# Kernel optimization log

Measured on AMD Instinct MI355X. Metric: run time of the kernel, lower is better.

Reference implementation:

```python
import jax, jax.numpy as jnp
from jax import lax
import numpy as np

NPOINT, RADIUS, NSAMPLE = 1024, 0.2, 32
MLP, IN_CH, EPS = (64, 64, 128), 6, 1e-5
B, N = 8, 4096


def farthest_point_sample(xyz, npoint):
    # xyz: [B, N, 3] -> idx [B, npoint]. Deterministic start at index 0.
    Bn, Nn, _ = xyz.shape
    def body(carry, _):
        dist, farthest = carry  # dist [B,N], farthest [B]
        centroid = jnp.take_along_axis(xyz, farthest[:, None, None], axis=1)  # [B,1,3]
        d = jnp.sum((xyz - centroid) ** 2, axis=-1)  # [B,N]
        dist = jnp.minimum(dist, d)
        return (dist, jnp.argmax(dist, axis=-1).astype(jnp.int32)), farthest
    init = (jnp.full((Bn, Nn), 1e10, xyz.dtype), jnp.zeros((Bn,), jnp.int32))
    _, idx = lax.scan(body, init, None, length=npoint)  # [npoint, B]
    return idx.T


def query_ball_point(radius, nsample, xyz, new_xyz):
    # xyz [B,N,3], new_xyz [B,S,3] -> idx [B,S,nsample]
    Bn, Nn, _ = xyz.shape
    sq = (jnp.sum(new_xyz ** 2, -1)[:, :, None]
          + jnp.sum(xyz ** 2, -1)[:, None, :]
          - 2.0 * jnp.einsum('bsc,bnc->bsn', new_xyz, xyz))  # [B,S,N]
    gidx = jnp.where(sq > radius ** 2, Nn, jnp.arange(Nn, dtype=jnp.int32)[None, None, :])
    gidx = jnp.sort(gidx, axis=-1)[:, :, :nsample]
    first = gidx[:, :, :1]
    return jnp.where(gidx == Nn, first, gidx)


def setup_inputs():
    key = jax.random.key(0)
    ks = jax.random.split(key, 8)
    inp = {
        'xyz': jax.random.uniform(ks[0], (B, 3, N), dtype=jnp.float32),
        'points': jax.random.normal(ks[1], (B, 3, N), dtype=jnp.float32),
    }
    last = IN_CH
    for i, oc in enumerate(MLP):
        inp[f'w{i}'] = jax.random.normal(ks[2 + i], (oc, last), dtype=jnp.float32) * 0.1
        inp[f'b{i}'] = jnp.zeros((oc,), jnp.float32)
        inp[f'g{i}'] = jnp.ones((oc,), jnp.float32)
        inp[f'be{i}'] = jnp.zeros((oc,), jnp.float32)
        last = oc
    return inp


def reference(xyz, points, w0, b0, g0, be0, w1, b1, g1, be1, w2, b2, g2, be2):
    x = jnp.transpose(xyz, (0, 2, 1))      # [B,N,3]
    p = jnp.transpose(points, (0, 2, 1))   # [B,N,D]
    fidx = farthest_point_sample(x, NPOINT)                       # [B,S]
    new_xyz = jnp.take_along_axis(x, fidx[:, :, None], axis=1)    # [B,S,3]
    idx = query_ball_point(RADIUS, NSAMPLE, x, new_xyz)           # [B,S,K]
    gather = jax.vmap(lambda a, i: a[i])                          # per-batch gather
    grouped_xyz = gather(x, idx)                                  # [B,S,K,3]
    grouped_xyz_norm = grouped_xyz - new_xyz[:, :, None, :]
    grouped_points = gather(p, idx)                               # [B,S,K,D]
    feat = jnp.concatenate([grouped_xyz_norm, grouped_points], axis=-1)  # [B,S,K,C]
    for w, b, g, be in ((w0, b0, g0, be0), (w1, b1, g1, be1), (w2, b2, g2, be2)):
        feat = jnp.einsum('bskc,oc->bsko', feat, w) + b
        mean = feat.mean(axis=(0, 1, 2))
        var = feat.var(axis=(0, 1, 2))
        feat = (feat - mean) * lax.rsqrt(var + EPS) * g + be  # BatchNorm (training stats)
        feat = jax.nn.relu(feat)
    new_points = jnp.max(feat, axis=2)                            # max over K -> [B,S,Cout]
    return jnp.transpose(new_xyz, (0, 2, 1)), jnp.transpose(new_points, (0, 2, 1))
```

## Files before the change

### kernel.cpp

```cpp
#include <hip/hip_runtime.h>
#include <stdint.h>

#define NPTS   4096
#define NPOINT 1024
#define NSAMP  32
#define NROWS  262144
#define RAD2   0.04f

typedef float v2f __attribute__((ext_vector_type(2)));
typedef __attribute__((ext_vector_type(8))) short bf16x8;
typedef __attribute__((ext_vector_type(4))) float f32x4;

__device__ __forceinline__ unsigned short f2bf(float x) {
    unsigned u = __float_as_uint(x);
    return (unsigned short)((u + 0x7FFFu + ((u >> 16) & 1u)) >> 16);
}
__device__ __forceinline__ unsigned pack2bf(float a, float b) {
    return (unsigned)f2bf(a) | ((unsigned)f2bf(b) << 16);
}

#define DPPMAX(v, C)                                                           \
    fmaxf(__int_as_float(__builtin_amdgcn_update_dpp(                          \
              0, __float_as_int(v), C, 0xf, 0xf, true)),                       \
          (v))

__global__ __launch_bounds__(256) void fps_kernel(const float* __restrict__ xyz,
                                                  float* __restrict__ outx)
{
    __shared__ __align__(16) float4 pxyz[NPTS];
    __shared__ __align__(16) float4 orec[NPOINT];
    __shared__ __align__(16) unsigned long long wkey[2][4];
    const int b = blockIdx.x, tid = threadIdx.x;
    const int lane = tid & 63, wid = tid >> 6;
    const float* base = xyz + b * 3 * NPTS;

    float Xs[16], Ys[16], Zs[16];
#pragma unroll
    for (int j = 0; j < 16; ++j) {
        const int n = j * 256 + tid;
        Xs[j] = base[n];
        Ys[j] = base[NPTS + n];
        Zs[j] = base[2 * NPTS + n];
        pxyz[n] = make_float4(Xs[j], Ys[j], Zs[j], 0.0f);
    }
    v2f X2[8], Y2[8], Z2[8], D2[8];
#pragma unroll
    for (int j = 0; j < 8; ++j) {
        X2[j] = (v2f){Xs[2 * j], Xs[2 * j + 1]};
        Y2[j] = (v2f){Ys[2 * j], Ys[2 * j + 1]};
        Z2[j] = (v2f){Zs[2 * j], Zs[2 * j + 1]};
        D2[j] = (v2f){1e10f, 1e10f};
    }
    __syncthreads();
    float4 c4 = pxyz[0];
    float cx = c4.x, cy = c4.y, cz = c4.z;

    for (int t = 0; t < NPOINT; ++t) {
        if (tid == 0) orec[t] = make_float4(cx, cy, cz, 0.0f);
        const v2f cxv = (v2f){cx, cx}, cyv = (v2f){cy, cy}, czv = (v2f){cz, cz};
        float bv = -1.0f; int bi = 0;
#pragma unroll
        for (int j = 0; j < 8; ++j) {
            v2f nd;
            {
#pragma clang fp contract(off)
                const v2f dx = X2[j] - cxv;
                const v2f dy = Y2[j] - cyv;
                const v2f dz = Z2[j] - czv;
                const v2f m0 = dx * dx;
                const v2f m1 = dy * dy;
                const v2f m2 = dz * dz;
                const v2f d = (m0 + m1) + m2;
                nd = __builtin_elementwise_min(D2[j], d);
            }
            D2[j] = nd;
            if (nd.x > bv) { bv = nd.x; bi = j * 512 + tid; }
            if (nd.y > bv) { bv = nd.y; bi = j * 512 + 256 + tid; }
        }
        float rv = bv;
        rv = DPPMAX(rv, 0x111);
        rv = DPPMAX(rv, 0x112);
        rv = DPPMAX(rv, 0x114);
        rv = DPPMAX(rv, 0x118);
        rv = DPPMAX(rv, 0x142);
        rv = DPPMAX(rv, 0x143);
        const unsigned wmax =
            (unsigned)__builtin_amdgcn_readlane(__float_as_int(rv), 63);
        unsigned long long mask = __ballot(__float_as_uint(bv) == wmax);
        unsigned best =
            (unsigned)__builtin_amdgcn_readlane(bi, (int)__builtin_ctzll(mask));
        mask &= mask - 1ull;
        while (mask) {
            const unsigned cand = (unsigned)__builtin_amdgcn_readlane(
                bi, (int)__builtin_ctzll(mask));
            best = cand < best ? cand : best;
            mask &= mask - 1ull;
        }
        if (lane == 0)
            wkey[t & 1][wid] = ((unsigned long long)wmax << 32) |
                               (unsigned)(~best);
        __syncthreads();
        const ulonglong2* wk = (const ulonglong2*)wkey[t & 1];
        const ulonglong2 ka = wk[0], kb = wk[1];
        unsigned long long kk = ka.x;
        if (ka.y > kk) kk = ka.y;
        if (kb.x > kk) kk = kb.x;
        if (kb.y > kk) kk = kb.y;
        const int farthest = (int)(~(unsigned)kk) & (NPTS - 1);
        c4 = pxyz[farthest];
        cx = c4.x; cy = c4.y; cz = c4.z;
    }
    __syncthreads();
    float* ox = outx + b * 3 * NPOINT;
    for (int i = tid; i < NPOINT; i += 256) {
        const float4 c = orec[i];
        ox[i]              = c.x;
        ox[NPOINT + i]     = c.y;
        ox[2 * NPOINT + i] = c.z;
    }
}

__global__ __launch_bounds__(256) void ball_kernel(const float* __restrict__ xyz,
                                                   const float* __restrict__ pts,
                                                   const float* __restrict__ outx,
                                                   float* __restrict__ mom,
                                                   uint4* __restrict__ featbuf)
{
    __shared__ float red[4][42];
    __shared__ int smyidx[4][NSAMP];
    const int tid = threadIdx.x;
    const int w = blockIdx.x * 4 + (tid >> 6);
    const int lane = tid & 63, wid = tid >> 6;
    const int b = w >> 10, s = w & 1023;
    const float* base = xyz + b * 3 * NPTS;
    const float cx = outx[b * 3 * NPOINT + s];
    const float cy = outx[b * 3 * NPOINT + NPOINT + s];
    const float cz = outx[b * 3 * NPOINT + 2 * NPOINT + s];
    const float sumS = __fadd_rn(__fadd_rn(__fmul_rn(cx, cx), __fmul_rn(cy, cy)),
                                 __fmul_rn(cz, cz));
    int cnt = 0, first_n = -1;
    int* myidx = smyidx[wid];

    for (int chunk = 0; chunk < NPTS / 64 && cnt < NSAMP; ++chunk) {
        const int n = chunk * 64 + lane;
        float nx = base[n], ny = base[NPTS + n], nz = base[2 * NPTS + n];
        float sumN = __fadd_rn(__fadd_rn(__fmul_rn(nx, nx), __fmul_rn(ny, ny)),
                               __fmul_rn(nz, nz));
        float dot = __fadd_rn(__fadd_rn(__fmul_rn(cx, nx), __fmul_rn(cy, ny)),
                              __fmul_rn(cz, nz));
        float sq = __fsub_rn(__fadd_rn(sumS, sumN), __fmul_rn(2.0f, dot));
        bool keep = (sq <= RAD2);
        unsigned long long mask = __ballot(keep);
        if (first_n < 0 && mask) first_n = chunk * 64 + (int)__builtin_ctzll(mask);
        int pos = cnt + __popcll(mask & ((1ull << lane) - 1ull));
        if (keep && pos < NSAMP) myidx[pos] = n;
        cnt += __popcll(mask);
    }
    if (cnt < NSAMP) {
        if (lane >= cnt && lane < NSAMP) myidx[lane] = first_n;
    }

    float m[42];
#pragma unroll
    for (int i = 0; i < 42; ++i) m[i] = 0.f;
    if (lane < 32) {
        const int idx = myidx[lane];
        const float* pb = pts + b * 3 * NPTS;
        float f[6];
        f[0] = base[idx] - cx;
        f[1] = base[NPTS + idx] - cy;
        f[2] = base[2 * NPTS + idx] - cz;
        f[3] = pb[idx];
        f[4] = pb[NPTS + idx];
        f[5] = pb[2 * NPTS + idx];
        featbuf[w * NSAMP + lane] =
            make_uint4(pack2bf(f[0], f[1]), pack2bf(f[2], f[3]),
                       pack2bf(f[4], f[5]), 0u);
#pragma unroll
        for (int c = 0; c < 6; ++c) m[c] = f[c];
#pragma unroll
        for (int c = 0; c < 6; ++c)
#pragma unroll
            for (int d = 0; d < 6; ++d)
                m[6 + c * 6 + d] = f[c] * f[d];
    }
#pragma unroll
    for (int i = 0; i < 42; ++i) {
        float v = m[i];
        v += __shfl_xor(v, 1);  v += __shfl_xor(v, 2);  v += __shfl_xor(v, 4);
        v += __shfl_xor(v, 8);  v += __shfl_xor(v, 16); v += __shfl_xor(v, 32);
        m[i] = v;
    }
    if (lane == 0) {
#pragma unroll
        for (int i = 0; i < 42; ++i) red[wid][i] = m[i];
    }
    __syncthreads();
    if (tid < 42)
        atomicAdd(&mom[tid], red[0][tid] + red[1][tid] + red[2][tid] + red[3][tid]);
}

__device__ __forceinline__ void compute_bn0(int o, const float* __restrict__ mom,
                                            const float* __restrict__ w0,
                                            const float* __restrict__ g,
                                            const float* __restrict__ be,
                                            float* __restrict__ sbn0)
{
    float w[6];
#pragma unroll
    for (int c = 0; c < 6; ++c) w[c] = w0[o * 6 + c];
    const float inv = 1.0f / (float)NROWS;
    float mean = 0.f;
#pragma unroll
    for (int c = 0; c < 6; ++c) mean = fmaf(w[c], mom[c], mean);
    mean *= inv;
    float ey2 = 0.f;
#pragma unroll
    for (int c = 0; c < 6; ++c) {
        float t = 0.f;
#pragma unroll
        for (int d = 0; d < 6; ++d) t = fmaf(w[d], mom[6 + c * 6 + d], t);
        ey2 = fmaf(w[c], t, ey2);
    }
    ey2 *= inv;
    const float var = ey2 - mean * mean;
    const float scale = g[o] * rsqrtf(var + 1e-5f);
    sbn0[o] = scale;
    sbn0[64 + o] = be[o] - mean * scale;
}

#define XP  72
#define WP  72
#define W0P 40

__global__ __launch_bounds__(256, 2) void mlp1_kernel(
    const uint4* __restrict__ featbuf,
    const float* __restrict__ w0, const float* __restrict__ mom,
    const float* __restrict__ g0, const float* __restrict__ be0,
    const float* __restrict__ w1, float* __restrict__ stats,
    uint4* __restrict__ l1store)
{
    __shared__ __align__(16) unsigned short sw0[64 * W0P];
    __shared__ __align__(16) unsigned short sw1[64 * WP];
    __shared__ __align__(16) unsigned short xb[4][32 * XP];
    __shared__ float sbn0[128];
    __shared__ float red[4][128];
    const int tid = threadIdx.x, lane = tid & 63, wid = tid >> 6;

    for (int i = tid; i < 64 * W0P / 2; i += 256) ((unsigned*)sw0)[i] = 0;
    if (tid < 64) compute_bn0(tid, mom, w0, g0, be0, sbn0);
    __syncthreads();
    for (int i = tid; i < 192; i += 256) {
        const int o = i / 3, c = (i % 3) * 2;
        *(unsigned*)&sw0[o * W0P + c] = pack2bf(w0[o * 6 + c], w0[o * 6 + c + 1]);
    }
    for (int i = tid; i < 2048; i += 256) {
        const int o = i >> 5, k = (i & 31) * 2;
        *(unsigned*)&sw1[o * WP + k] = pack2bf(w1[o * 64 + k], w1[o * 64 + k + 1]);
    }

    const int mh = lane & 15, q = lane >> 4;
    unsigned short* X = xb[wid];
    const int rbase = blockIdx.x * 512 + wid * 32;
    float sA[4] = {0.f, 0.f, 0.f, 0.f}, qA[4] = {0.f, 0.f, 0.f, 0.f};

    for (int c = 0; c < 4; ++c) {
        __syncthreads();
        if (lane < 32) {
            const int r = rbase + c * 128 + lane;
            uint4* xq = (uint4*)&xb[wid][lane * XP];
            xq[0] = featbuf[r];
            xq[1] = make_uint4(0u, 0u, 0u, 0u);
            xq[2] = make_uint4(0u, 0u, 0u, 0u);
            xq[3] = make_uint4(0u, 0u, 0u, 0u);
        }
        __syncthreads();
        f32x4 acc0[2][4] = {};
        {
            bf16x8 a[2], bw[4];
#pragma unroll
            for (int mt = 0; mt < 2; ++mt)
                a[mt] = *(const bf16x8*)&X[(mt * 16 + mh) * XP + q * 8];
#pragma unroll
            for (int nt = 0; nt < 4; ++nt)
                bw[nt] = *(const bf16x8*)&sw0[(nt * 16 + mh) * W0P + q * 8];
#pragma unroll
            for (int mt = 0; mt < 2; ++mt)
#pragma unroll
                for (int nt = 0; nt < 4; ++nt)
                    acc0[mt][nt] = __builtin_amdgcn_mfma_f32_16x16x32_bf16(
                        a[mt], bw[nt], acc0[mt][nt], 0, 0, 0);
        }
        __syncthreads();
#pragma unroll
        for (int nt = 0; nt < 4; ++nt) {
            const int ch = nt * 16 + mh;
            const float sc = sbn0[ch], sh = sbn0[64 + ch];
#pragma unroll
            for (int mt = 0; mt < 2; ++mt)
#pragma unroll
                for (int rr = 0; rr < 4; ++rr) {
                    const float v = fmaxf(fmaf(acc0[mt][nt][rr], sc, sh), 0.0f);
                    X[(mt * 16 + q * 4 + rr) * XP + ch] = f2bf(v);
                }
        }
        __syncthreads();
        f32x4 acc1[2][4] = {};
#pragma unroll
        for (int ks = 0; ks < 2; ++ks) {
            bf16x8 a[2], bw[4];
#pragma unroll
            for (int mt = 0; mt < 2; ++mt)
                a[mt] = *(const bf16x8*)&X[(mt * 16 + mh) * XP + ks * 32 + q * 8];
#pragma unroll
            for (int nt = 0; nt < 4; ++nt)
                bw[nt] = *(const bf16x8*)&sw1[(nt * 16 + mh) * WP + ks * 32 + q * 8];
#pragma unroll
            for (int mt = 0; mt < 2; ++mt)
#pragma unroll
                for (int nt = 0; nt < 4; ++nt)
                    acc1[mt][nt] = __builtin_amdgcn_mfma_f32_16x16x32_bf16(
                        a[mt], bw[nt], acc1[mt][nt], 0, 0, 0);
        }
#pragma unroll
        for (int nt = 0; nt < 4; ++nt)
#pragma unroll
            for (int mt = 0; mt < 2; ++mt)
#pragma unroll
                for (int rr = 0; rr < 4; ++rr) {
                    const float v = acc1[mt][nt][rr];
                    sA[nt] += v;
                    qA[nt] = fmaf(v, v, qA[nt]);
                }
        if (l1store) {
#pragma unroll
            for (int nt = 0; nt < 4; ++nt) {
                const int ch = nt * 16 + mh;
#pragma unroll
                for (int mt = 0; mt < 2; ++mt)
#pragma unroll
                    for (int rr = 0; rr < 4; ++rr)
                        X[(mt * 16 + q * 4 + rr) * XP + ch] =
                            f2bf(acc1[mt][nt][rr]);
            }
            uint4* dst = l1store +
                         (size_t)(blockIdx.x * 16 + c * 4 + wid) * 256;
#pragma unroll
            for (int k = 0; k < 4; ++k) {
                const int idx = lane * 4 + k;
                const int row = idx >> 3, c8 = (idx & 7) * 8;
                dst[idx] = *(const uint4*)&X[row * XP + c8];
            }
        }
    }
#pragma unroll
    for (int nt = 0; nt < 4; ++nt) {
        float s = sA[nt], qq = qA[nt];
        s += __shfl_xor(s, 16); qq += __shfl_xor(qq, 16);
        s += __shfl_xor(s, 32); qq += __shfl_xor(qq, 32);
        if (q == 0) {
            red[wid][nt * 16 + mh] = s;
            red[wid][64 + nt * 16 + mh] = qq;
        }
    }
    __syncthreads();
    if (tid < 128)
        atomicAdd(&stats[tid],
                  red[0][tid] + red[1][tid] + red[2][tid] + red[3][tid]);
}

__global__ __launch_bounds__(256, 2) void mlp2b_kernel(
    const uint4* __restrict__ l1buf,
    const float* __restrict__ stats1,
    const float* __restrict__ g1, const float* __restrict__ be1,
    const float* __restrict__ w2,
    float* __restrict__ stats, float* __restrict__ gmax)
{
    __shared__ __align__(16) unsigned short sw2[128 * WP];
    __shared__ float sbn1[128];
    __shared__ float red[4][256];
    const int tid = threadIdx.x, lane = tid & 63, wid = tid >> 6;

    if (tid < 64) {
        const float inv = 1.0f / (float)NROWS;
        const float mean = stats1[tid] * inv;
        const float var = stats1[64 + tid] * inv - mean * mean;
        const float scale = g1[tid] * rsqrtf(var + 1e-5f);
        sbn1[tid] = scale;
        sbn1[64 + tid] = be1[tid] - mean * scale;
    }
    for (int i = tid; i < 4096; i += 256) {
        const int o = i >> 5, k = (i & 31) * 2;
        *(unsigned*)&sw2[o * WP + k] = pack2bf(w2[o * 64 + k], w2[o * 64 + k + 1]);
    }
    __syncthreads();

    const int mh = lane & 15, q = lane >> 4;
    float sc[2][8], sh[2][8];
#pragma unroll
    for (int ks = 0; ks < 2; ++ks)
#pragma unroll
        for (int j = 0; j < 8; ++j) {
            const int ch = ks * 32 + q * 8 + j;
            sc[ks][j] = sbn1[ch];
            sh[ks][j] = sbn1[64 + ch];
        }

    float sA[8], qA[8];
#pragma unroll
    for (int i = 0; i < 8; ++i) { sA[i] = 0.f; qA[i] = 0.f; }

    for (int c = 0; c < 4; ++c) {
        const int g = blockIdx.x * 16 + c * 4 + wid;
        const uint4* src = l1buf + (size_t)g * 256;
        bf16x8 a2[2][2];
#pragma unroll
        for (int mt = 0; mt < 2; ++mt)
#pragma unroll
            for (int ks = 0; ks < 2; ++ks) {
                const int row = mt * 16 + mh;
                const uint4 v = src[row * 8 + ks * 4 + q];
                const unsigned* pv = (const unsigned*)&v;
                unsigned r[4];
#pragma unroll
                for (int p = 0; p < 4; ++p) {
                    const unsigned u = pv[p];
                    const float f0 = __uint_as_float(u << 16);
                    const float f1 = __uint_as_float(u & 0xFFFF0000u);
                    const float v0 =
                        fmaxf(fmaf(f0, sc[ks][2 * p], sh[ks][2 * p]), 0.0f);
                    const float v1 =
                        fmaxf(fmaf(f1, sc[ks][2 * p + 1], sh[ks][2 * p + 1]),
                              0.0f);
                    r[p] = pack2bf(v0, v1);
                }
                const uint4 packed = make_uint4(r[0], r[1], r[2], r[3]);
                a2[mt][ks] = __builtin_bit_cast(bf16x8, packed);
            }
#pragma unroll
        for (int nt = 0; nt < 8; ++nt) {
            f32x4 acc[2] = {};
#pragma unroll
            for (int ks = 0; ks < 2; ++ks) {
                const bf16x8 bw =
                    *(const bf16x8*)&sw2[(nt * 16 + mh) * WP + ks * 32 + q * 8];
#pragma unroll
                for (int mt = 0; mt < 2; ++mt)
                    acc[mt] = __builtin_amdgcn_mfma_f32_16x16x32_bf16(
                        a2[mt][ks], bw, acc[mt], 0, 0, 0);
            }
            float m = -3.0e38f;
#pragma unroll
            for (int mt = 0; mt < 2; ++mt)
#pragma unroll
                for (int rr = 0; rr < 4; ++rr) {
                    const float v = acc[mt][rr];
                    sA[nt] += v;
                    qA[nt] = fmaf(v, v, qA[nt]);
                    m = fmaxf(m, v);
                }
            m = fmaxf(m, __shfl_xor(m, 16));
            m = fmaxf(m, __shfl_xor(m, 32));
            if (q == 0) gmax[(nt * 16 + mh) * 8192 + g] = m;
        }
    }
#pragma unroll
    for (int nt = 0; nt < 8; ++nt) {
        float s = sA[nt], qq = qA[nt];
        s += __shfl_xor(s, 16); qq += __shfl_xor(qq, 16);
        s += __shfl_xor(s, 32); qq += __shfl_xor(qq, 32);
        if (q == 0) {
            red[wid][nt * 16 + mh] = s;
            red[wid][128 + nt * 16 + mh] = qq;
        }
    }
    __syncthreads();
    atomicAdd(&stats[tid],
              red[0][tid] + red[1][tid] + red[2][tid] + red[3][tid]);
}

__global__ __launch_bounds__(256, 2) void mlp2_kernel(
    const uint4* __restrict__ featbuf,
    const float* __restrict__ w0, const float* __restrict__ mom,
    const float* __restrict__ g0, const float* __restrict__ be0,
    const float* __restrict__ w1, const float* __restrict__ stats1,
    const float* __restrict__ g1, const float* __restrict__ be1,
    const float* __restrict__ w2,
    float* __restrict__ stats, float* __restrict__ gmax)
{
    __shared__ __align__(16) unsigned short sw0[64 * W0P];
    __shared__ __align__(16) unsigned short sw1[64 * WP];
    __shared__ __align__(16) unsigned short sw2[128 * WP];
    __shared__ __align__(16) unsigned short xb[4][32 * XP];
    __shared__ float sbn0[128];
    __shared__ float sbn1[128];
    __shared__ float red[4][256];
    const int tid = threadIdx.x, lane = tid & 63, wid = tid >> 6;

    for (int i = tid; i < 64 * W0P / 2; i += 256) ((unsigned*)sw0)[i] = 0;
    if (tid < 64) {
        compute_bn0(tid, mom, w0, g0, be0, sbn0);
    } else if (tid < 128) {
        const int ch = tid - 64;
        const float inv = 1.0f / (float)NROWS;
        const float mean = stats1[ch] * inv;
        const float var = stats1[64 + ch] * inv - mean * mean;
        const float scale = g1[ch] * rsqrtf(var + 1e-5f);
        sbn1[ch] = scale;
        sbn1[64 + ch] = be1[ch] - mean * scale;
    }
    __syncthreads();
    for (int i = tid; i < 192; i += 256) {
        const int o = i / 3, c = (i % 3) * 2;
        *(unsigned*)&sw0[o * W0P + c] = pack2bf(w0[o * 6 + c], w0[o * 6 + c + 1]);
    }
    for (int i = tid; i < 2048; i += 256) {
        const int o = i >> 5, k = (i & 31) * 2;
        *(unsigned*)&sw1[o * WP + k] = pack2bf(w1[o * 64 + k], w1[o * 64 + k + 1]);
    }
    for (int i = tid; i < 4096; i += 256) {
        const int o = i >> 5, k = (i & 31) * 2;
        *(unsigned*)&sw2[o * WP + k] = pack2bf(w2[o * 64 + k], w2[o * 64 + k + 1]);
    }

    const int mh = lane & 15, q = lane >> 4;
    unsigned short* X = xb[wid];
    const int rbase = blockIdx.x * 512 + wid * 32;
    float sA[8], qA[8];
#pragma unroll
    for (int i = 0; i < 8; ++i) { sA[i] = 0.f; qA[i] = 0.f; }

    for (int c = 0; c < 4; ++c) {
        __syncthreads();
        if (lane < 32) {
            const int r = rbase + c * 128 + lane;
            uint4* xq = (uint4*)&xb[wid][lane * XP];
            xq[0] = featbuf[r];
            xq[1] = make_uint4(0u, 0u, 0u, 0u);
            xq[2] = make_uint4(0u, 0u, 0u, 0u);
            xq[3] = make_uint4(0u, 0u, 0u, 0u);
        }
        __syncthreads();
        f32x4 acc0[2][4] = {};
        {
            bf16x8 a[2], bw[4];
#pragma unroll
            for (int mt = 0; mt < 2; ++mt)
                a[mt] = *(const bf16x8*)&X[(mt * 16 + mh) * XP + q * 8];
#pragma unroll
            for (int nt = 0; nt < 4; ++nt)
                bw[nt] = *(const bf16x8*)&sw0[(nt * 16 + mh) * W0P + q * 8];
#pragma unroll
            for (int mt = 0; mt < 2; ++mt)
#pragma unroll
                for (int nt = 0; nt < 4; ++nt)
                    acc0[mt][nt] = __builtin_amdgcn_mfma_f32_16x16x32_bf16(
                        a[mt], bw[nt], acc0[mt][nt], 0, 0, 0);
        }
        __syncthreads();
#pragma unroll
        for (int nt = 0; nt < 4; ++nt) {
            const int ch = nt * 16 + mh;
            const float sc = sbn0[ch], sh = sbn0[64 + ch];
#pragma unroll
            for (int mt = 0; mt < 2; ++mt)
#pragma unroll
                for (int rr = 0; rr < 4; ++rr) {
                    const float v = fmaxf(fmaf(acc0[mt][nt][rr], sc, sh), 0.0f);
                    X[(mt * 16 + q * 4 + rr) * XP + ch] = f2bf(v);
                }
        }
        __syncthreads();
        f32x4 acc1[2][4] = {};
#pragma unroll
        for (int ks = 0; ks < 2; ++ks) {
            bf16x8 a[2], bw[4];
#pragma unroll
            for (int mt = 0; mt < 2; ++mt)
                a[mt] = *(const bf16x8*)&X[(mt * 16 + mh) * XP + ks * 32 + q * 8];
#pragma unroll
            for (int nt = 0; nt < 4; ++nt)
                bw[nt] = *(const bf16x8*)&sw1[(nt * 16 + mh) * WP + ks * 32 + q * 8];
#pragma unroll
            for (int mt = 0; mt < 2; ++mt)
#pragma unroll
                for (int nt = 0; nt < 4; ++nt)
                    acc1[mt][nt] = __builtin_amdgcn_mfma_f32_16x16x32_bf16(
                        a[mt], bw[nt], acc1[mt][nt], 0, 0, 0);
        }
        __syncthreads();
#pragma unroll
        for (int nt = 0; nt < 4; ++nt) {
            const int ch = nt * 16 + mh;
            const float sc = sbn1[ch], sh = sbn1[64 + ch];
#pragma unroll
            for (int mt = 0; mt < 2; ++mt)
#pragma unroll
                for (int rr = 0; rr < 4; ++rr) {
                    const float v = fmaxf(fmaf(acc1[mt][nt][rr], sc, sh), 0.0f);
                    X[(mt * 16 + q * 4 + rr) * XP + ch] = f2bf(v);
                }
        }
        __syncthreads();
        const int g = blockIdx.x * 16 + c * 4 + wid;
        bf16x8 a2[2][2];
#pragma unroll
        for (int mt = 0; mt < 2; ++mt)
#pragma unroll
            for (int ks = 0; ks < 2; ++ks)
                a2[mt][ks] = *(const bf16x8*)&X[(mt * 16 + mh) * XP + ks * 32 + q * 8];
#pragma unroll
        for (int nt = 0; nt < 8; ++nt) {
            f32x4 acc[2] = {};
#pragma unroll
            for (int ks = 0; ks < 2; ++ks) {
                const bf16x8 bw = *(const bf16x8*)&sw2[(nt * 16 + mh) * WP + ks * 32 + q * 8];
#pragma unroll
                for (int mt = 0; mt < 2; ++mt)
                    acc[mt] = __builtin_amdgcn_mfma_f32_16x16x32_bf16(
                        a2[mt][ks], bw, acc[mt], 0, 0, 0);
            }
            float m = -3.0e38f;
#pragma unroll
            for (int mt = 0; mt < 2; ++mt)
#pragma unroll
                for (int rr = 0; rr < 4; ++rr) {
                    const float v = acc[mt][rr];
                    sA[nt] += v;
                    qA[nt] = fmaf(v, v, qA[nt]);
                    m = fmaxf(m, v);
                }
            m = fmaxf(m, __shfl_xor(m, 16));
            m = fmaxf(m, __shfl_xor(m, 32));
            if (q == 0) gmax[(nt * 16 + mh) * 8192 + g] = m;
        }
    }
#pragma unroll
    for (int nt = 0; nt < 8; ++nt) {
        float s = sA[nt], qq = qA[nt];
        s += __shfl_xor(s, 16); qq += __shfl_xor(qq, 16);
        s += __shfl_xor(s, 32); qq += __shfl_xor(qq, 32);
        if (q == 0) {
            red[wid][nt * 16 + mh] = s;
            red[wid][128 + nt * 16 + mh] = qq;
        }
    }
    __syncthreads();
    atomicAdd(&stats[tid],
              red[0][tid] + red[1][tid] + red[2][tid] + red[3][tid]);
}

__global__ __launch_bounds__(256) void final_kernel(const float* __restrict__ gmax,
                                                    const float* __restrict__ stats2,
                                                    const float* __restrict__ g2,
                                                    const float* __restrict__ be2,
                                                    float* __restrict__ out2)
{
    __shared__ float sbn[256];
    const int tid = threadIdx.x;
    if (tid < 128) {
        const float inv = 1.0f / (float)NROWS;
        const float mean = stats2[tid] * inv;
        const float var = stats2[128 + tid] * inv - mean * mean;
        const float scale = g2[tid] * rsqrtf(var + 1e-5f);
        sbn[tid] = scale;
        sbn[128 + tid] = be2[tid] - mean * scale;
    }
    __syncthreads();
    const int t = blockIdx.x * 256 + tid;
    const int s = t & 1023;
    const int o = (t >> 10) & 127;
    const int b = t >> 17;
    const int g = (b << 10) | s;
    float v = gmax[o * 8192 + g];
    v = fmaf(v, sbn[o], sbn[128 + o]);
    out2[t] = fmaxf(v, 0.0f);
}

extern "C" void kernel_launch(void* const* d_in, const int* in_sizes, int n_in,
                              void* d_out, int out_size, void* d_ws, size_t ws_size,
                              hipStream_t stream)
{
    const float* xyz = (const float*)d_in[0];
    const float* pts = (const float*)d_in[1];
    const float* w0  = (const float*)d_in[2];
    const float* g0  = (const float*)d_in[4];
    const float* be0 = (const float*)d_in[5];
    const float* w1  = (const float*)d_in[6];
    const float* g1  = (const float*)d_in[8];
    const float* be1 = (const float*)d_in[9];
    const float* w2  = (const float*)d_in[10];
    const float* g2  = (const float*)d_in[12];
    const float* be2 = (const float*)d_in[13];

    float* out_xyz = (float*)d_out;
    float* out2    = out_xyz + 8 * 3 * NPOINT;

    char* wsb = (char*)d_ws;
    float* stats   = (float*)(wsb + 32768 + 1048576);
    float* gmax    = stats + 1024;
    uint4* featbuf = (uint4*)(gmax + 128 * 8192);
    uint4* l1buf   = featbuf + NROWS;

    float* mom    = stats;
    float* stats1 = stats + 128;
    float* stats2 = stats + 256;

    const bool bigws = ws_size >= (size_t)43100000;

    hipMemsetAsync(stats, 0, 512 * sizeof(float), stream);

    fps_kernel<<<8, 256, 0, stream>>>(xyz, out_xyz);
    ball_kernel<<<2048, 256, 0, stream>>>(xyz, pts, out_xyz, mom, featbuf);
    if (bigws) {
        mlp1_kernel<<<512, 256, 0, stream>>>(featbuf, w0, mom, g0, be0,
                                             w1, stats1, l1buf);
        mlp2b_kernel<<<512, 256, 0, stream>>>(l1buf, stats1, g1, be1,
                                              w2, stats2, gmax);
    } else {
        mlp1_kernel<<<512, 256, 0, stream>>>(featbuf, w0, mom, g0, be0,
                                             w1, stats1, nullptr);
        mlp2_kernel<<<512, 256, 0, stream>>>(featbuf, w0, mom, g0, be0,
                                             w1, stats1, g1, be1,
                                             w2, stats2, gmax);
    }
    final_kernel<<<4096, 256, 0, stream>>>(gmax, stats2, g2, be2, out2);
}
```

Baseline: 793.3 us.

## Prefetch next chunk loads, use DPP reductions, drop block barriers in MLP loop

The ball-query loop now prefetches the next 64-point chunk's coordinates into registers so global-load latency overlaps the distance test and ballot. The 42-value moment reduction swaps four shuffle-xor steps for DPP row operations. The MLP kernel prefetches the next featbuf tile into a register and replaces the per-iteration __syncthreads calls with one barrier after the weight setup, since each wave works only on its own staging buffer. Removing the barriers assumes same-wave LDS ordering is enough, and the DPP pattern has to reproduce the original butterfly sums exactly.

```diff
diff --git a/kernel.cpp b/kernel.cpp
--- a/kernel.cpp
+++ b/kernel.cpp
@@ -23,6 +23,10 @@
     fmaxf(__int_as_float(__builtin_amdgcn_update_dpp(                          \
               0, __float_as_int(v), C, 0xf, 0xf, true)),                       \
           (v))
+#define DPPADD(v, C)                                                           \
+    (__int_as_float(__builtin_amdgcn_update_dpp(                               \
+         0, __float_as_int(v), C, 0xf, 0xf, true)) +                           \
+     (v))
 
 __global__ __launch_bounds__(256) void fps_kernel(const float* __restrict__ xyz,
                                                   float* __restrict__ outx)
@@ -141,13 +145,18 @@
     int cnt = 0, first_n = -1;
     int* myidx = smyidx[wid];
 
+    float nx = base[lane], ny = base[NPTS + lane], nz = base[2 * NPTS + lane];
     for (int chunk = 0; chunk < NPTS / 64 && cnt < NSAMP; ++chunk) {
+        const float x = nx, y = ny, z = nz;
+        if (chunk + 1 < NPTS / 64) {
+            const int nn = (chunk + 1) * 64 + lane;
+            nx = base[nn]; ny = base[NPTS + nn]; nz = base[2 * NPTS + nn];
+        }
         const int n = chunk * 64 + lane;
-        float nx = base[n], ny = base[NPTS + n], nz = base[2 * NPTS + n];
-        float sumN = __fadd_rn(__fadd_rn(__fmul_rn(nx, nx), __fmul_rn(ny, ny)),
-                               __fmul_rn(nz, nz));
-        float dot = __fadd_rn(__fadd_rn(__fmul_rn(cx, nx), __fmul_rn(cy, ny)),
-                              __fmul_rn(cz, nz));
+        float sumN = __fadd_rn(__fadd_rn(__fmul_rn(x, x), __fmul_rn(y, y)),
+                               __fmul_rn(z, z));
+        float dot = __fadd_rn(__fadd_rn(__fmul_rn(cx, x), __fmul_rn(cy, y)),
+                              __fmul_rn(cz, z));
         float sq = __fsub_rn(__fadd_rn(sumS, sumN), __fmul_rn(2.0f, dot));
         bool keep = (sq <= RAD2);
         unsigned long long mask = __ballot(keep);
@@ -187,8 +196,11 @@
 #pragma unroll
     for (int i = 0; i < 42; ++i) {
         float v = m[i];
-        v += __shfl_xor(v, 1);  v += __shfl_xor(v, 2);  v += __shfl_xor(v, 4);
-        v += __shfl_xor(v, 8);  v += __shfl_xor(v, 16); v += __shfl_xor(v, 32);
+        v = DPPADD(v, 0x111);
+        v = DPPADD(v, 0x112);
+        v = DPPADD(v, 0x114);
+        v = DPPADD(v, 0x118);
+        v += __shfl_xor(v, 16);
         m[i] = v;
     }
     if (lane == 0) {
@@ -258,23 +270,25 @@
         const int o = i >> 5, k = (i & 31) * 2;
         *(unsigned*)&sw1[o * WP + k] = pack2bf(w1[o * 64 + k], w1[o * 64 + k + 1]);
     }
+    __syncthreads();
 
     const int mh = lane & 15, q = lane >> 4;
     unsigned short* X = xb[wid];
     const int rbase = blockIdx.x * 512 + wid * 32;
     float sA[4] = {0.f, 0.f, 0.f, 0.f}, qA[4] = {0.f, 0.f, 0.f, 0.f};
 
+    uint4 preg = make_uint4(0u, 0u, 0u, 0u);
+    if (lane < 32) preg = featbuf[rbase + lane];
+
     for (int c = 0; c < 4; ++c) {
-        __syncthreads();
         if (lane < 32) {
-            const int r = rbase + c * 128 + lane;
             uint4* xq = (uint4*)&xb[wid][lane * XP];
-            xq[0] = featbuf[r];
+            xq[0] = preg;
             xq[1] = make_uint4(0u, 0u, 0u, 0u);
             xq[2] = make_uint4(0u, 0u, 0u, 0u);
             xq[3] = make_uint4(0u, 0u, 0u, 0u);
-        }
-        __syncthreads();
+            if (c < 3) preg = featbuf[rbase + (c + 1) * 128 + lane];
+        }
         f32x4 acc0[2][4] = {};
         {
             bf16x8 a[2], bw[4];
@@ -291,7 +305,6 @@
                     acc0[mt][nt] = __builtin_amdgcn_mfma_f32_16x16x32_bf16(
                         a[mt], bw[nt], acc0[mt][nt], 0, 0, 0);
         }
-        __syncthreads();
 #pragma unroll
         for (int nt = 0; nt < 4; ++nt) {
             const int ch = nt * 16 + mh;
@@ -304,7 +317,6 @@
                     X[(mt * 16 + q * 4 + rr) * XP + ch] = f2bf(v);
                 }
         }
-        __syncthreads();
         f32x4 acc1[2][4] = {};
 #pragma unroll
         for (int ks = 0; ks < 2; ++ks) {
```

New measurement: 774.3 us. -2.4%, faster.
